# Performance work log

Hardware: AMD Instinct MI355X
Metric: run time of the kernel (lower is better)

The kernel has to match this reference:

```python
import jax, jax.numpy as jnp
import numpy as np

K = 5          # kernel_size per dim
B = 100        # batch size (hard-coded in source)
GRID = 28
NUM_FIRST_FC = 49  # adjs[2].size(0) = 7*7


def spline_conv(x, edge_index, pseudo, W, root, bias):
    """Degree-1 open B-spline graph conv (SplineGCN).
    x: [N, Cin]; edge_index: [2, E] (src, dst); pseudo: [E, 2] in [0,1];
    W: [K*K, Cin, Cout]; root: [Cin, Cout]; bias: [Cout].
    out_i = mean_{j->i} sum_taps b_tap(u_ij) * (x_j @ W[k_tap]) + x_i @ root + bias
    """
    N = x.shape[0]
    src, dst = edge_index[0], edge_index[1]
    pos = pseudo * (K - 1)                     # open spline: scale to [0, K-1]
    kf = jnp.floor(pos)
    frac = pos - kf                            # [E, 2]
    k0 = kf.astype(jnp.int32)
    k1 = jnp.minimum(k0 + 1, K - 1)
    # Precompute x @ W[k] for all 25 kernel indices: [N, K*K, Cout]
    y = jnp.einsum('ni,kio->nko', x, W)
    fx, fy = frac[:, 0], frac[:, 1]
    taps = [
        (k0[:, 0], k0[:, 1], (1 - fx) * (1 - fy)),
        (k0[:, 0], k1[:, 1], (1 - fx) * fy),
        (k1[:, 0], k0[:, 1], fx * (1 - fy)),
        (k1[:, 0], k1[:, 1], fx * fy),
    ]
    msg = jnp.zeros((src.shape[0], W.shape[2]), dtype=x.dtype)
    for ax, ay, w in taps:
        msg = msg + w[:, None] * y[src, ax * K + ay]   # gather [E, Cout]
    agg = jax.ops.segment_sum(msg, dst, num_segments=N)
    deg = jax.ops.segment_sum(jnp.ones_like(msg[:, 0]), dst, num_segments=N)
    return agg / jnp.maximum(deg, 1.0)[:, None] + x @ root + bias


def max_pool2(x):  # x: [b, H, W, C] -> [b, H/2, W/2, C] (same math as NCHW pool)
    b, h, w, c = x.shape
    return x.reshape(b, h // 2, 2, w // 2, 2, c).max(axis=(2, 4))


def setup_inputs() -> dict:
    key = jax.random.key(0)
    ks = jax.random.split(key, 16)
    N0, N1 = B * GRID * GRID, B * (GRID // 2) * (GRID // 2)
    E0, E1 = N0 * 8, N1 * 8
    s = 0.1
    return {
        'x': jax.random.normal(ks[0], (N0, 1), dtype=jnp.float32),
        'pseudo0': jax.random.uniform(ks[1], (E0, 2), dtype=jnp.float32),
        'pseudo1': jax.random.uniform(ks[2], (E1, 2), dtype=jnp.float32),
        'W1': jax.random.normal(ks[3], (K * K, 1, 32), dtype=jnp.float32) * s,
        'root1': jax.random.normal(ks[4], (1, 32), dtype=jnp.float32) * s,
        'b1': jnp.zeros((32,), dtype=jnp.float32),
        'W2': jax.random.normal(ks[5], (K * K, 32, 64), dtype=jnp.float32) * s,
        'root2': jax.random.normal(ks[6], (32, 64), dtype=jnp.float32) * s,
        'b2': jnp.zeros((64,), dtype=jnp.float32),
        'fc1_w': jax.random.normal(ks[7], (NUM_FIRST_FC * 64, 512), dtype=jnp.float32) * 0.02,
        'fc1_b': jnp.zeros((512,), dtype=jnp.float32),
        'fc2_w': jax.random.normal(ks[8], (512, 10), dtype=jnp.float32) * 0.02,
        'fc2_b': jnp.zeros((10,), dtype=jnp.float32),
        'edge_index0': jax.random.randint(ks[9], (2, E0), 0, N0, dtype=jnp.int32),
        'edge_index1': jax.random.randint(ks[10], (2, E1), 0, N1, dtype=jnp.int32),
    }


def reference(x, pseudo0, pseudo1, W1, root1, b1, W2, root2, b2,
              fc1_w, fc1_b, fc2_w, fc2_b, edge_index0, edge_index1):
    elu = jax.nn.elu
    # conv1 on 28x28 grid graph
    h = elu(spline_conv(x, edge_index0, pseudo0, W1, root1, b1))   # [B*784, 32]
    h = h.reshape(-1, GRID, GRID, 32)                              # [B, 28, 28, 32]
    h = max_pool2(h)                                               # [B, 14, 14, 32]
    h = h.reshape(-1, 32)                                          # [B*196, 32]
    # conv2 on 14x14 grid graph
    h = elu(spline_conv(h, edge_index1, pseudo1, W2, root2, b2))   # [B*196, 64]
    # faithful replication of the source's reshapes: (B*196) rows -> (B/4, 28, 28, 64)
    h = h.reshape(-1, GRID, GRID, 64)                              # [25, 28, 28, 64]
    h = max_pool2(h)                                               # [25, 14, 14, 64]
    h = h.reshape(-1, NUM_FIRST_FC * 64)                           # [100, 3136]
    h = elu(h @ fc1_w + fc1_b)
    # F.dropout with training=False (eval) is identity
    h = elu(h @ fc2_w + fc2_b)
    return jax.nn.log_softmax(h, axis=-1)
```

## Files before the change

kernel.cpp:

```cpp
#include <hip/hip_runtime.h>
#include <hip/hip_bf16.h>

#define KK 5
constexpr int N0 = 78400;
constexpr int E0 = 627200;
constexpr int N1 = 19600;
constexpr int E1 = 156800;
constexpr int C1 = 32, C2 = 64;
constexpr int BSZ = 100;
constexpr int FC1_IN = 3136, FC1_OUT = 512;
constexpr int NKEYS = 98000;
constexpr int NCOARSE = 383;
constexpr int CAPB = 2400;
constexpr int KEXT = 832;
constexpr int ULS = 836;
constexpr int UBS = 856;
constexpr int CH2 = 160;
constexpr int CH1 = 640;

typedef __attribute__((ext_vector_type(8))) short bf16x8;
typedef __attribute__((ext_vector_type(4))) float f32x4;

__device__ __forceinline__ unsigned short f2bf(float f) {
    union { float f; unsigned u; } v; v.f = f;
    unsigned u = v.u;
    unsigned r = (u + 0x7FFF + ((u >> 16) & 1)) >> 16;
    return (unsigned short)r;
}

__device__ __forceinline__ void taps4(float px, float py,
                                      int& a00, int& a01, int& a10, int& a11,
                                      float& fx, float& fy) {
    float kfx = floorf(px), kfy = floorf(py);
    fx = px - kfx; fy = py - kfy;
    int k0x = min(max((int)kfx, 0), KK - 1);
    int k0y = min(max((int)kfy, 0), KK - 1);
    int k1x = min(k0x + 1, KK - 1), k1y = min(k0y + 1, KK - 1);
    a00 = k0x * KK + k0y; a01 = k0x * KK + k1y;
    a10 = k1x * KK + k0y; a11 = k1x * KK + k1y;
}

__global__ void coarse_bin(const int* __restrict__ ei0, const int* __restrict__ ei1,
                           int* __restrict__ gcur, int* __restrict__ pk,
                           const float* __restrict__ fc1w, const float* __restrict__ W2,
                           const float* __restrict__ root2,
                           unsigned short* __restrict__ wt1,
                           unsigned short* __restrict__ w2t) {
    __shared__ int hist[NCOARSE];
    __shared__ int gbase[NCOARSE];
    __shared__ unsigned short tile[64 * 66];
    int t = threadIdx.x;
    if (blockIdx.x >= 192) {
        int pb = blockIdx.x - 192;
        if (pb >= 392) {
            int base = (pb - 392) * 6656;
            for (int i2 = t; i2 < 6656; i2 += 512) {
                int idx = base + i2;
                int o = idx / KEXT, k = idx - o * KEXT;
                float v = (k < 800) ? W2[k * 64 + o] : root2[(k - 800) * 64 + o];
                w2t[idx] = f2bf(v);
            }
            return;
        }
        int k0 = (pb >> 3) * 64, j0 = (pb & 7) * 64;
        int jj = t & 63, ks = t >> 6;
        for (int kk = ks; kk < 64; kk += 8)
            tile[kk * 66 + jj] = f2bf(fc1w[(k0 + kk) * FC1_OUT + j0 + jj]);
        __syncthreads();
        int kk2 = t & 63, js = t >> 6;
        for (int j2 = js; j2 < 64; j2 += 8)
            wt1[(j0 + j2) * FC1_IN + k0 + kk2] = tile[kk2 * 66 + j2];
        return;
    }
    for (int i = t; i < NCOARSE; i += 512) hist[i] = 0;
    __syncthreads();
    int e0b = blockIdx.x * 4096;
    int ids[8], keys[8], rnk[8];
#pragma unroll
    for (int j = 0; j < 8; j++) {
        int e = e0b + t + j * 512;
        int gk = -1, id = 0;
        if (e < E0) { gk = ei0[E0 + e]; id = e; }
        else if (e < E0 + E1) { int el = e - E0; gk = N0 + ei1[E1 + el]; id = el; }
        ids[j] = id; keys[j] = gk;
    }
#pragma unroll
    for (int j = 0; j < 8; j++)
        if (keys[j] >= 0) rnk[j] = atomicAdd(&hist[keys[j] >> 8], 1);
    __syncthreads();
    for (int i = t; i < NCOARSE; i += 512)
        gbase[i] = hist[i] ? atomicAdd(&gcur[i], hist[i]) : 0;
    __syncthreads();
#pragma unroll
    for (int j = 0; j < 8; j++) {
        if (keys[j] >= 0) {
            int b = keys[j] >> 8;
            int p = gbase[b] + rnk[j];
            if (p < CAPB) pk[b * CAPB + p] = ids[j] | ((keys[j] & 255) << 20);
        }
    }
}

__global__ void fine_sort(const int* __restrict__ pk, const int* __restrict__ gcur,
                          int* __restrict__ idxx, int* __restrict__ off) {
    __shared__ int cl[NCOARSE];
    __shared__ int ent[CAPB];
    __shared__ int rnk[CAPB];
    __shared__ int h2[256];
    __shared__ int sc[256];
    __shared__ int redbuf[4];
    __shared__ int baseS;
    int b = blockIdx.x, t = threadIdx.x;
    for (int i2 = t; i2 < NCOARSE; i2 += 256) cl[i2] = min(gcur[i2], CAPB);
    __syncthreads();
    {
        int s = 0;
        if (t < b) s += cl[t];
        if (t + 256 < b) s += cl[t + 256];
#pragma unroll
        for (int o2 = 32; o2 > 0; o2 >>= 1) s += __shfl_down(s, o2);
        if ((t & 63) == 0) redbuf[t >> 6] = s;
        __syncthreads();
        if (t == 0) baseS = redbuf[0] + redbuf[1] + redbuf[2] + redbuf[3];
        __syncthreads();
    }
    int base = baseS;
    int cb = cl[b];
    h2[t] = 0;
    __syncthreads();
    for (int i = t; i < cb; i += 256) {
        int v = pk[b * CAPB + i];
        ent[i] = v;
        rnk[i] = atomicAdd(&h2[(v >> 20) & 255], 1);
    }
    __syncthreads();
    int v0 = h2[t];
    sc[t] = v0;
    __syncthreads();
    for (int d = 1; d < 256; d <<= 1) {
        int add = (t >= d) ? sc[t - d] : 0;
        __syncthreads();
        sc[t] += add;
        __syncthreads();
    }
    int excl = sc[t] - v0;
    __syncthreads();
    sc[t] = excl;
    __syncthreads();
    int n = (b << 8) + t;
    if (n < NKEYS) off[n] = base + excl;
    if (b == 0 && t == 0) off[NKEYS] = E0 + E1;
    for (int i = t; i < cb; i += 256) {
        int v = ent[i];
        idxx[base + sc[(v >> 20) & 255] + rnk[i]] = v & 0xFFFFF;
    }
}

__global__ __launch_bounds__(256, 4)
void conv1_pool(const int* __restrict__ idxx, const int* __restrict__ off,
                const float* __restrict__ x, const int* __restrict__ ei0,
                const float* __restrict__ ps0, const float* __restrict__ W1,
                const float* __restrict__ root, const float* __restrict__ bias,
                float* __restrict__ p1) {
    __shared__ float S4[224 * 25];
    __shared__ float Sr[56 * 25];
    __shared__ float exv[CH1], efx[CH1], efy[CH1];
    __shared__ int   emt[CH1];
    float* h1t = S4;
    int t = threadIdx.x;
    int bb = blockIdx.x;
    int n0 = bb * 56;
    int q = t & 3, nl = t >> 2;
    bool actN = nl < 56;
    int n = n0 + (actN ? nl : 0);
    float* sp = S4 + (actN ? (nl * 4 + q) : 0) * 25;
    for (int i = t; i < 224 * 25; i += 256) S4[i] = 0.f;
    int e0 = off[n0], e1 = off[n0 + 56];
    int my0 = off[n], my1 = off[n + 1];
    for (int base = e0; base < e1; base += CH1) {
        int nE = min(e1 - base, CH1);
        __syncthreads();
        for (int j = t; j < nE; j += 256) {
            int e = idxx[base + j];
            int src = ei0[e];
            int a00, a01, a10, a11; float fx, fy;
            taps4(ps0[2 * e] * (KK - 1), ps0[2 * e + 1] * (KK - 1),
                  a00, a01, a10, a11, fx, fy);
            emt[j] = a00 | (a01 << 5) | (a10 << 10) | (a11 << 15);
            efx[j] = fx; efy[j] = fy;
            exv[j] = x[src];
        }
        __syncthreads();
        if (actN) {
            int r0 = max(my0 - base, 0), r1 = min(my1 - base, nE);
            for (int p = r0 + q; p < r1; p += 4) {
                float xv = exv[p]; int m = emt[p];
                float fx = efx[p], fy = efy[p];
                float gx = 1.f - fx, gy = 1.f - fy;
                sp[m & 31]         += gx * gy * xv;
                sp[(m >> 5) & 31]  += gx * fy * xv;
                sp[(m >> 10) & 31] += fx * gy * xv;
                sp[(m >> 15) & 31] += fx * fy * xv;
            }
        }
    }
    __syncthreads();
    for (int i2 = t; i2 < 56 * 25; i2 += 256) {
        int n2 = i2 / 25, a = i2 - n2 * 25;
        Sr[i2] = S4[(n2 * 4 + 0) * 25 + a] + S4[(n2 * 4 + 1) * 25 + a] +
                 S4[(n2 * 4 + 2) * 25 + a] + S4[(n2 * 4 + 3) * 25 + a];
    }
    __syncthreads();
    {
        int o = t & 31, ng = t >> 5;
        float w1c[25];
#pragma unroll
        for (int a = 0; a < 25; a++) w1c[a] = W1[a * C1 + o];
        float ro = root[o], bo = bias[o];
        for (int j2 = 0; j2 < 7; j2++) {
            int nl2 = ng * 7 + j2;
            int n2 = n0 + nl2;
            float acc = 0.f;
#pragma unroll
            for (int a = 0; a < 25; a++) acc += Sr[nl2 * 25 + a] * w1c[a];
            float invd = 1.f / fmaxf((float)(off[n2 + 1] - off[n2]), 1.f);
            float v = acc * invd + x[n2] * ro + bo;
            h1t[nl2 * 32 + o] = v > 0.f ? v : expm1f(v);
        }
    }
    __syncthreads();
    for (int i2 = t; i2 < 448; i2 += 256) {
        int o2 = i2 & 31, pc = i2 >> 5;
        float m0 = h1t[(2 * pc) * 32 + o2],      m1 = h1t[(2 * pc + 1) * 32 + o2];
        float m2 = h1t[(28 + 2 * pc) * 32 + o2], m3 = h1t[(28 + 2 * pc + 1) * 32 + o2];
        p1[(bb * 14 + pc) * C1 + o2] = fmaxf(fmaxf(m0, m1), fmaxf(m2, m3));
    }
}

__global__ __launch_bounds__(256, 5)
void conv2_fused(const float* __restrict__ p1, const int* __restrict__ idxx,
                 const int* __restrict__ off, const int* __restrict__ ei1,
                 const float* __restrict__ ps1,
                 const unsigned short* __restrict__ w2t,
                 const float* __restrict__ b2, float* __restrict__ h2) {
    __shared__ float Ul[8 * ULS];
    __shared__ int   es[CH2];
    __shared__ int   et[CH2];
    __shared__ float efx[CH2], efy[CH2];
    unsigned short* Ub = (unsigned short*)Ul;
    int t = threadIdx.x;
    int nb = blockIdx.x * 8;
    int i = t & 31, g = t >> 5;
    float* up = Ul + g * ULS;
#pragma unroll
    for (int a = 0; a < 25; a++) up[a * 32 + i] = 0.f;
    up[800 + i] = p1[(nb + g) * C1 + i];
    int e0 = off[N0 + nb], e1 = off[N0 + nb + 8];
    int my0 = off[N0 + nb + g], my1 = off[N0 + nb + g + 1];
    for (int base = e0; base < e1; base += CH2) {
        int nE = min(e1 - base, CH2);
        __syncthreads();
        for (int j = t; j < nE; j += 256) {
            int e = idxx[base + j];
            es[j] = ei1[e];
            int a00, a01, a10, a11; float fx, fy;
            taps4(ps1[2 * e] * (KK - 1), ps1[2 * e + 1] * (KK - 1),
                  a00, a01, a10, a11, fx, fy);
            et[j] = a00 | (a01 << 5) | (a10 << 10) | (a11 << 15);
            efx[j] = fx; efy[j] = fy;
        }
        __syncthreads();
        int r0 = max(my0 - base, 0);
        int r1 = min(my1 - base, nE);
        int myT = max(r1 - r0, 0);
        int m64 = max(myT, __shfl_xor(myT, 32));
        for (int jj = 0; jj < m64; jj += 2) {
            bool a0 = jj < myT, a1 = jj + 1 < myT;
            int j0 = a0 ? r0 + jj : 0, j1 = a1 ? r0 + jj + 1 : 0;
            int s0 = es[j0], s1 = es[j1];
            int mm0 = et[j0], mm1 = et[j1];
            float fx0 = efx[j0], fy0 = efy[j0];
            float fx1 = efx[j1], fy1 = efy[j1];
            float x0 = p1[s0 * C1 + i];
            float x1 = p1[s1 * C1 + i];
            if (a0) {
                float gx = 1.f - fx0, gy = 1.f - fy0;
                up[(mm0 & 31) * 32 + i]         += gx * gy * x0;
                up[((mm0 >> 5) & 31) * 32 + i]  += gx * fy0 * x0;
                up[((mm0 >> 10) & 31) * 32 + i] += fx0 * gy * x0;
                up[((mm0 >> 15) & 31) * 32 + i] += fx0 * fy0 * x0;
            }
            if (a1) {
                float gx = 1.f - fx1, gy = 1.f - fy1;
                up[(mm1 & 31) * 32 + i]         += gx * gy * x1;
                up[((mm1 >> 5) & 31) * 32 + i]  += gx * fy1 * x1;
                up[((mm1 >> 10) & 31) * 32 + i] += fx1 * gy * x1;
                up[((mm1 >> 15) & 31) * 32 + i] += fx1 * fy1 * x1;
            }
        }
    }
    __syncthreads();
    {
        int g2 = t >> 5, ks = (t & 31) * 26;
        int dgc = off[N0 + nb + g2 + 1] - off[N0 + nb + g2];
        float invd = 1.f / fmaxf((float)dgc, 1.f);
        const float* srcp = Ul + g2 * ULS + ks;
        float rv[26];
#pragma unroll
        for (int j = 0; j < 26; j++) {
            float v = srcp[j];
            rv[j] = (ks + j < 800) ? v * invd : v;
        }
        __syncthreads();
        unsigned* dstp = (unsigned*)(Ub + g2 * UBS + ks);
#pragma unroll
        for (int j = 0; j < 13; j++) {
            unsigned lo = f2bf(rv[2 * j]), hi = f2bf(rv[2 * j + 1]);
            dstp[j] = lo | (hi << 16);
        }
    }
    __syncthreads();
    int wv = t >> 6, lane = t & 63, quad = lane >> 4, lrow = lane & 15;
    f32x4 acc = {0.f, 0.f, 0.f, 0.f};
    int nodeA = lrow & 7;
    const unsigned short* bbase = w2t + (wv * 16 + lrow) * KEXT;
    const unsigned short* abase = Ub + nodeA * UBS;
#pragma unroll
    for (int kc = 0; kc < 26; kc++) {
        bf16x8 a = *(const bf16x8*)(abase + kc * 32 + quad * 8);
        bf16x8 b = *(const bf16x8*)(bbase + kc * 32 + quad * 8);
        acc = __builtin_amdgcn_mfma_f32_16x16x32_bf16(a, b, acc, 0, 0, 0);
    }
    if (quad < 2) {
        int o = wv * 16 + lrow;
        float bo = b2[o];
#pragma unroll
        for (int r = 0; r < 4; r++) {
            int node = quad * 4 + r;
            float v = acc[r] + bo;
            v = v > 0.f ? v : expm1f(v);
            h2[(nb + node) * C2 + o] = v;
        }
    }
}

__global__ void pool2b(const float* __restrict__ h2, unsigned short* __restrict__ p2b) {
    int idx = blockIdx.x * blockDim.x + threadIdx.x;
    if (idx >= 112 * FC1_IN) return;
    if (idx >= 100 * FC1_IN) { p2b[idx] = 0; return; }
    int o = idx & 63; int t2 = idx >> 6;
    int c = t2 % 14; int r = (t2 / 14) % 14; int b = t2 / 196;
    const float* base = h2 + (((b * 28 + 2 * r) * 28 + 2 * c) * C2 + o);
    float m = fmaxf(fmaxf(base[0], base[C2]),
                    fmaxf(base[28 * C2], base[28 * C2 + C2]));
    p2b[idx] = f2bf(m);
}

__global__ void gemm_fc1(const unsigned short* __restrict__ p2b,
                         const unsigned short* __restrict__ wt1,
                         float* __restrict__ z1p) {
    constexpr int AS = 232;
    __shared__ unsigned short as_[16 * AS];
    int t = threadIdx.x;
    int jt = blockIdx.x, mt = blockIdx.y, kz = blockIdx.z;
    int wv = t >> 6, lane = t & 63, quad = lane >> 4, lrow = lane & 15;
    int m0 = mt * 16;
    int kbase = kz * 1568;
    const unsigned short* bbase = wt1 + (jt * 64 + wv * 16 + lrow) * FC1_IN + kbase;
    f32x4 acc = {0.f, 0.f, 0.f, 0.f};
    for (int ch = 0; ch < 7; ch++) {
        __syncthreads();
        for (int slot = t; slot < 448; slot += 256) {
            int r = slot / 28, c = slot - (slot / 28) * 28;
            *(uint4*)(as_ + r * AS + c * 8) =
                *(const uint4*)(p2b + (m0 + r) * FC1_IN + kbase + ch * 224 + c * 8);
        }
        __syncthreads();
        const unsigned short* ab = as_ + lrow * AS;
        const unsigned short* bb = bbase + ch * 224;
#pragma unroll
        for (int kk = 0; kk < 7; kk++) {
            bf16x8 a = *(const bf16x8*)(ab + kk * 32 + quad * 8);
            bf16x8 b = *(const bf16x8*)(bb + kk * 32 + quad * 8);
            acc = __builtin_amdgcn_mfma_f32_16x16x32_bf16(a, b, acc, 0, 0, 0);
        }
    }
    int n = jt * 64 + wv * 16 + lrow;
#pragma unroll
    for (int r = 0; r < 4; r++) {
        int m = m0 + quad * 4 + r;
        z1p[kz * (112 * FC1_OUT) + m * FC1_OUT + n] = acc[r];
    }
}

__global__ void fc2_lsm(const float* __restrict__ z1p, const float* __restrict__ fc1b,
                        const float* __restrict__ w, const float* __restrict__ fc2b,
                        float* __restrict__ out) {
    int b = blockIdx.x;
    int t = threadIdx.x;
    int wv = t >> 6;
    int lane = t & 63;
    float acc = 0.f;
#pragma unroll
    for (int m = 0; m < 8; m++) {
        int k = lane * 8 + m;
        float xv = fc1b[k] + z1p[b * FC1_OUT + k] + z1p[112 * FC1_OUT + b * FC1_OUT + k];
        xv = xv > 0.f ? xv : expm1f(xv);
        acc += xv * w[k * 10 + wv];
    }
#pragma unroll
    for (int off = 32; off > 0; off >>= 1) acc += __shfl_down(acc, off);
    __shared__ float zs[10];
    if (lane == 0) {
        float z = acc + fc2b[wv];
        zs[wv] = z > 0.f ? z : expm1f(z);
    }
    __syncthreads();
    if (t < 10) {
        float m = -1e30f;
        for (int jj = 0; jj < 10; jj++) m = fmaxf(m, zs[jj]);
        float s = 0.f;
        for (int jj = 0; jj < 10; jj++) s += expf(zs[jj] - m);
        out[b * 10 + t] = zs[t] - m - logf(s);
    }
}

extern "C" void kernel_launch(void* const* d_in, const int* in_sizes, int n_in,
                              void* d_out, int out_size, void* d_ws, size_t ws_size,
                              hipStream_t stream) {
    const float* x     = (const float*)d_in[0];
    const float* ps0   = (const float*)d_in[1];
    const float* ps1   = (const float*)d_in[2];
    const float* W1    = (const float*)d_in[3];
    const float* root1 = (const float*)d_in[4];
    const float* b1    = (const float*)d_in[5];
    const float* W2    = (const float*)d_in[6];
    const float* root2 = (const float*)d_in[7];
    const float* b2v   = (const float*)d_in[8];
    const float* fc1w  = (const float*)d_in[9];
    const float* fc1b  = (const float*)d_in[10];
    const float* fc2w  = (const float*)d_in[11];
    const float* fc2b  = (const float*)d_in[12];
    const int*   ei0   = (const int*)d_in[13];
    const int*   ei1   = (const int*)d_in[14];

    float* ws = (float*)d_ws;
    int* gcur  = (int*)ws;
    int* off   = (int*)(ws + 384);
    int* pk    = (int*)(ws + 98388);
    int* idxx  = (int*)(ws + 1017588);
    float* p1  = ws + 1801588;
    float* h2  = ws + 2428788;
    unsigned short* p2b = (unsigned short*)(ws + 3683188);
    float* z1p = ws + 3858804;
    unsigned short* w2t = (unsigned short*)(ws + 3973492);
    unsigned short* wt1 = (unsigned short*)(ws + 4000116);

    hipMemsetAsync(gcur, 0, (size_t)NCOARSE * sizeof(int), stream);

    coarse_bin<<<592, 512, 0, stream>>>(ei0, ei1, gcur, pk, fc1w, W2, root2, wt1, w2t);
    fine_sort<<<NCOARSE, 256, 0, stream>>>(pk, gcur, idxx, off);
    conv1_pool<<<1400, 256, 0, stream>>>(idxx, off, x, ei0, ps0,
                                         W1, root1, b1, p1);
    conv2_fused<<<N1 / 8, 256, 0, stream>>>(p1, idxx, off, ei1, ps1, w2t, b2v, h2);
    pool2b<<<(112 * FC1_IN + 255) / 256, 256, 0, stream>>>(h2, p2b);
    gemm_fc1<<<dim3(8, 7, 2), 256, 0, stream>>>(p2b, wt1, z1p);
    fc2_lsm<<<BSZ, 640, 0, stream>>>(z1p, fc1b, fc2w, fc2b, (float*)d_out);
}
```

Measured before the change: 219.7 us.

## Split conv2 edge accumulation across two warps per node with 4-edge unroll

conv2_fused now handles 4 destination nodes per block instead of 8, giving each node two 32-lane slices that take alternating edges into separate LDS partial accumulators. The partials are summed during the bf16 conversion step. The edge loop is also unrolled to four edges per iteration so more gathers are in flight. This shortens the per-node serial scatter-add chain and doubles the grid size, at the cost of the MFMA stage computing only 4 useful rows of 16, which doubles the total MFMA and weight-load work.

```diff
diff --git a/kernel.cpp b/kernel.cpp
--- a/kernel.cpp
+++ b/kernel.cpp
@@ -249,13 +249,15 @@
     __shared__ float efx[CH2], efy[CH2];
     unsigned short* Ub = (unsigned short*)Ul;
     int t = threadIdx.x;
-    int nb = blockIdx.x * 8;
-    int i = t & 31, g = t >> 5;
-    float* up = Ul + g * ULS;
+    int nb = blockIdx.x * 4;
+    int i = t & 31;
+    int sl = t >> 5;
+    int g = sl >> 1, s = sl & 1;
+    float* up = Ul + sl * ULS;
 #pragma unroll
     for (int a = 0; a < 25; a++) up[a * 32 + i] = 0.f;
-    up[800 + i] = p1[(nb + g) * C1 + i];
-    int e0 = off[N0 + nb], e1 = off[N0 + nb + 8];
+    up[800 + i] = s ? 0.f : p1[(nb + g) * C1 + i];
+    int e0 = off[N0 + nb], e1 = off[N0 + nb + 4];
     int my0 = off[N0 + nb + g], my1 = off[N0 + nb + g + 1];
     for (int base = e0; base < e1; base += CH2) {
         int nE = min(e1 - base, CH2);
@@ -272,17 +274,25 @@
         __syncthreads();
         int r0 = max(my0 - base, 0);
         int r1 = min(my1 - base, nE);
-        int myT = max(r1 - r0, 0);
-        int m64 = max(myT, __shfl_xor(myT, 32));
-        for (int jj = 0; jj < m64; jj += 2) {
-            bool a0 = jj < myT, a1 = jj + 1 < myT;
-            int j0 = a0 ? r0 + jj : 0, j1 = a1 ? r0 + jj + 1 : 0;
-            int s0 = es[j0], s1 = es[j1];
-            int mm0 = et[j0], mm1 = et[j1];
+        int len = max(r1 - r0, 0);
+        int cnt = (len + 1 - s) >> 1;
+        int m4 = max(cnt, __shfl_xor(cnt, 32));
+        for (int jj = 0; jj < m4; jj += 4) {
+            bool a0 = jj < cnt, a1 = jj + 1 < cnt, a2 = jj + 2 < cnt, a3 = jj + 3 < cnt;
+            int j0 = a0 ? r0 + s + 2 * jj       : 0;
+            int j1 = a1 ? r0 + s + 2 * (jj + 1) : 0;
+            int j2 = a2 ? r0 + s + 2 * (jj + 2) : 0;
+            int j3 = a3 ? r0 + s + 2 * (jj + 3) : 0;
+            int s0 = es[j0], s1 = es[j1], s2 = es[j2], s3 = es[j3];
+            int mm0 = et[j0], mm1 = et[j1], mm2 = et[j2], mm3 = et[j3];
             float fx0 = efx[j0], fy0 = efy[j0];
             float fx1 = efx[j1], fy1 = efy[j1];
+            float fx2 = efx[j2], fy2 = efy[j2];
+            float fx3 = efx[j3], fy3 = efy[j3];
             float x0 = p1[s0 * C1 + i];
             float x1 = p1[s1 * C1 + i];
+            float x2 = p1[s2 * C1 + i];
+            float x3 = p1[s3 * C1 + i];
             if (a0) {
                 float gx = 1.f - fx0, gy = 1.f - fy0;
                 up[(mm0 & 31) * 32 + i]         += gx * gy * x0;
@@ -297,32 +307,52 @@
                 up[((mm1 >> 10) & 31) * 32 + i] += fx1 * gy * x1;
                 up[((mm1 >> 15) & 31) * 32 + i] += fx1 * fy1 * x1;
             }
+            if (a2) {
+                float gx = 1.f - fx2, gy = 1.f - fy2;
+                up[(mm2 & 31) * 32 + i]         += gx * gy * x2;
+                up[((mm2 >> 5) & 31) * 32 + i]  += gx * fy2 * x2;
+                up[((mm2 >> 10) & 31) * 32 + i] += fx2 * gy * x2;
+                up[((mm2 >> 15) & 31) * 32 + i] += fx2 * fy2 * x2;
+            }
+            if (a3) {
+                float gx = 1.f - fx3, gy = 1.f - fy3;
+                up[(mm3 & 31) * 32 + i]         += gx * gy * x3;
+                up[((mm3 >> 5) & 31) * 32 + i]  += gx * fy3 * x3;
+                up[((mm3 >> 10) & 31) * 32 + i] += fx3 * gy * x3;
+                up[((mm3 >> 15) & 31) * 32 + i] += fx3 * fy3 * x3;
+            }
         }
     }
     __syncthreads();
     {
-        int g2 = t >> 5, ks = (t & 31) * 26;
-        int dgc = off[N0 + nb + g2 + 1] - off[N0 + nb + g2];
-        float invd = 1.f / fmaxf((float)dgc, 1.f);
-        const float* srcp = Ul + g2 * ULS + ks;
+        int g2 = t >> 5, i2c = t & 31;
+        bool act = g2 < 4;
         float rv[26];
-#pragma unroll
-        for (int j = 0; j < 26; j++) {
-            float v = srcp[j];
-            rv[j] = (ks + j < 800) ? v * invd : v;
-        }
-        __syncthreads();
-        unsigned* dstp = (unsigned*)(Ub + g2 * UBS + ks);
-#pragma unroll
-        for (int j = 0; j < 13; j++) {
-            unsigned lo = f2bf(rv[2 * j]), hi = f2bf(rv[2 * j + 1]);
-            dstp[j] = lo | (hi << 16);
+        if (act) {
+            int dgc = off[N0 + nb + g2 + 1] - off[N0 + nb + g2];
+            float invd = 1.f / fmaxf((float)dgc, 1.f);
+            const float* sA = Ul + (2 * g2) * ULS + i2c * 26;
+            const float* sB = sA + ULS;
+#pragma unroll
+            for (int j = 0; j < 26; j++) {
+                float v = sA[j] + sB[j];
+                rv[j] = (i2c * 26 + j < 800) ? v * invd : v;
+            }
+        }
+        __syncthreads();
+        if (act) {
+            unsigned* dstp = (unsigned*)(Ub + g2 * UBS + i2c * 26);
+#pragma unroll
+            for (int j = 0; j < 13; j++) {
+                unsigned lo = f2bf(rv[2 * j]), hi = f2bf(rv[2 * j + 1]);
+                dstp[j] = lo | (hi << 16);
+            }
         }
     }
     __syncthreads();
     int wv = t >> 6, lane = t & 63, quad = lane >> 4, lrow = lane & 15;
     f32x4 acc = {0.f, 0.f, 0.f, 0.f};
-    int nodeA = lrow & 7;
+    int nodeA = lrow & 3;
     const unsigned short* bbase = w2t + (wv * 16 + lrow) * KEXT;
     const unsigned short* abase = Ub + nodeA * UBS;
 #pragma unroll
@@ -331,15 +361,14 @@
         bf16x8 b = *(const bf16x8*)(bbase + kc * 32 + quad * 8);
         acc = __builtin_amdgcn_mfma_f32_16x16x32_bf16(a, b, acc, 0, 0, 0);
     }
-    if (quad < 2) {
+    if (quad == 0) {
         int o = wv * 16 + lrow;
         float bo = b2[o];
 #pragma unroll
         for (int r = 0; r < 4; r++) {
-            int node = quad * 4 + r;
             float v = acc[r] + bo;
             v = v > 0.f ? v : expm1f(v);
-            h2[(nb + node) * C2 + o] = v;
+            h2[(nb + r) * C2 + o] = v;
         }
     }
 }
@@ -462,7 +491,7 @@
     fine_sort<<<NCOARSE, 256, 0, stream>>>(pk, gcur, idxx, off);
     conv1_pool<<<1400, 256, 0, stream>>>(idxx, off, x, ei0, ps0,
                                          W1, root1, b1, p1);
-    conv2_fused<<<N1 / 8, 256, 0, stream>>>(p1, idxx, off, ei1, ps1, w2t, b2v, h2);
+    conv2_fused<<<N1 / 4, 256, 0, stream>>>(p1, idxx, off, ei1, ps1, w2t, b2v, h2);
     pool2b<<<(112 * FC1_IN + 255) / 256, 256, 0, stream>>>(h2, p2b);
     gemm_fc1<<<dim3(8, 7, 2), 256, 0, stream>>>(p2b, wt1, z1p);
     fc2_lsm<<<BSZ, 640, 0, stream>>>(z1p, fc1b, fc2w, fc2b, (float*)d_out);
```

New measurement: 248.5 us. +13.1%, slower.
